# Performance work log

Hardware: AMD Instinct MI355X
Metric: run time of the kernel (lower is better)

The kernel has to match this reference:

```python
import jax, jax.numpy as jnp
import numpy as np

B, T, K, D, H, HL, S, KN = 4096, 50, 32, 64, 256, 128, 100000, 1000


def setup_inputs() -> dict:
    key = jax.random.key(0)
    ks = jax.random.split(key, 24)
    inp = {
        "uididx": jax.random.randint(ks[0], (B,), 0, S, dtype=jnp.int32),
        "kcodeidx": jax.random.randint(ks[1], (B, K), 0, KN, dtype=jnp.int32),
        "kcode_len": jax.random.randint(ks[2], (B,), 1, K + 1, dtype=jnp.int32),
        "qidemb": jax.random.normal(ks[3], (B, T, D), dtype=jnp.float32),
        "qid_len": jax.random.randint(ks[4], (B,), 1, T + 1, dtype=jnp.int32),
        # embedding tables
        "stuE": jax.random.normal(ks[5], (S, D), dtype=jnp.float32) * 0.1,
        "knE": jax.random.normal(ks[6], (KN, D), dtype=jnp.float32) * 0.1,
        # Theta DNN params
        "T_W1": jax.random.normal(ks[7], (D, H), dtype=jnp.float32) * (1.0 / np.sqrt(D)),
        "T_b1": jnp.zeros((H,), jnp.float32),
        "T_W2": jax.random.normal(ks[8], (H, 1), dtype=jnp.float32) * (1.0 / np.sqrt(H)),
        "T_b2": jnp.zeros((1,), jnp.float32),
        # A DNN params
        "A_W1": jax.random.normal(ks[9], (D, H), dtype=jnp.float32) * (1.0 / np.sqrt(D)),
        "A_b1": jnp.zeros((H,), jnp.float32),
        "A_W2": jax.random.normal(ks[10], (H, 1), dtype=jnp.float32) * (1.0 / np.sqrt(H)),
        "A_b2": jnp.zeros((1,), jnp.float32),
        # LSTM params (gate order i,f,g,o) + output head
        "L_Wi": jax.random.normal(ks[11], (D, 4 * HL), dtype=jnp.float32) * (1.0 / np.sqrt(D)),
        "L_Wh": jax.random.normal(ks[12], (HL, 4 * HL), dtype=jnp.float32) * (1.0 / np.sqrt(HL)),
        "L_b": jnp.zeros((4 * HL,), jnp.float32),
        "L_Wo": jax.random.normal(ks[13], (HL, 1), dtype=jnp.float32) * (1.0 / np.sqrt(HL)),
        "L_bo": jnp.zeros((1,), jnp.float32),
    }
    return inp


def _dnn(x, W1, b1, W2, b2):
    return jnp.tanh(x @ W1 + b1) @ W2 + b2


def _lstm_last(x, lengths, Wi, Wh, b):
    # x: [B,T,D]; returns last valid hidden state [B,HL]
    xg = jnp.einsum('btd,dh->bth', x, Wi) + b  # precomputed input projections
    h0 = jnp.zeros((x.shape[0], Wh.shape[0]), x.dtype)

    def step(carry, inp):
        h, c = carry
        g_x, t = inp
        g = g_x + h @ Wh
        i, f, gg, o = jnp.split(g, 4, axis=-1)
        c2 = jax.nn.sigmoid(f) * c + jax.nn.sigmoid(i) * jnp.tanh(gg)
        h2 = jax.nn.sigmoid(o) * jnp.tanh(c2)
        upd = (t < lengths)[:, None]
        return (jnp.where(upd, h2, h), jnp.where(upd, c2, c)), None

    (h, _), _ = jax.lax.scan(step, (h0, h0), (xg.transpose(1, 0, 2), jnp.arange(x.shape[1])))
    return h


def reference(uididx, kcodeidx, kcode_len, qidemb, qid_len, stuE, knE,
              T_W1, T_b1, T_W2, T_b2, A_W1, A_b1, A_W2, A_b2,
              L_Wi, L_Wh, L_b, L_Wo, L_bo):
    stu = stuE[uididx]            # [B,D]
    kemb = knE[kcodeidx]          # [B,K,D]
    kmask = jnp.arange(kcodeidx.shape[1])[None, :] < kcode_len[:, None]  # [B,K]
    kmf = kmask.astype(kemb.dtype)

    # per-student mastery: sigmoid(kemb @ stu / 5), then masked reductions
    mastery = jax.nn.sigmoid(jnp.einsum('bkd,bd->bk', kemb, stu) / 5.0)
    mastvec = jnp.einsum('bk,bkd->bd', mastery * kmf, kemb)  # sum(mastery * kemb)
    avec = jnp.einsum('bk,bkd->bd', kmf, kemb)               # sum(kemb)

    # scaled dot-product attention: q=qidemb, k=v=kemb, scale=0.15
    scores = jnp.einsum('btd,bkd->btk', qidemb, kemb) * 0.15
    scores = jnp.where(kmask[:, None, :], scores, -1e9)
    attw = jax.nn.softmax(scores, axis=-1)
    bvec = jnp.einsum('btk,bkd->btd', attw, kemb)            # [B,T,D]

    t = _dnn(mastvec, T_W1, T_b1, T_W2, T_b2)                             # theta [B,1]
    a = 8.0 * (jax.nn.sigmoid(jnp.abs(_dnn(avec, A_W1, A_b1, A_W2, A_b2))) - 0.5)
    hT = _lstm_last(bvec, qid_len, L_Wi, L_Wh, L_b)
    b = 8.0 * (jax.nn.sigmoid(hT @ L_Wo + L_bo) - 0.5)                    # [B,1]

    return jax.nn.sigmoid(a * (t - b))  # IRT response probability [B,1]
```

## Files before the change

### kernel.cpp

```cpp
#include <hip/hip_runtime.h>
#include <math.h>

#define B_  4096
#define T_  50
#define K_  32
#define D_  64
#define H_  256
#define HL_ 128
#define G4_ 512

typedef __attribute__((ext_vector_type(8))) short bf16x8;
typedef __attribute__((ext_vector_type(4))) float f32x4;

__device__ __forceinline__ float fast_exp(float x){ return __expf(x); }
__device__ __forceinline__ float fast_rcp(float x){ return __builtin_amdgcn_rcpf(x); }
__device__ __forceinline__ float sigmoidf_(float x){ return fast_rcp(1.f + fast_exp(-x)); }
__device__ __forceinline__ float tanhf_(float x){ return 1.f - 2.f*fast_rcp(1.f + fast_exp(2.f*x)); }

__device__ __forceinline__ short f2bf(float f){
  union { float f; unsigned u; } v; v.f = f;
  unsigned r = v.u + 0x7FFFu + ((v.u >> 16) & 1u);
  return (short)(r >> 16);
}
__device__ __forceinline__ float bf2f(short s){
  union { unsigned u; float f; } v; v.u = ((unsigned)(unsigned short)s) << 16;
  return v.f;
}

__device__ __forceinline__ float wave_reduce_sum(float v){
  #pragma unroll
  for (int off = 32; off; off >>= 1) v += __shfl_xor(v, off);
  return v;
}

#define KROW 72
#define PROW 40

__global__ __launch_bounds__(256) void head_kernel(
    const int* __restrict__ uididx, const int* __restrict__ kcodeidx,
    const int* __restrict__ kcode_len, const float* __restrict__ qidemb,
    const int* __restrict__ qid_len, const float* __restrict__ stuE,
    const float* __restrict__ knE,
    const float* __restrict__ T_W1, const float* __restrict__ T_b1,
    const float* __restrict__ T_W2, const float* __restrict__ T_b2,
    const float* __restrict__ A_W1, const float* __restrict__ A_b1,
    const float* __restrict__ A_W2, const float* __restrict__ A_b2,
    short* __restrict__ bvec, float* __restrict__ t_val, float* __restrict__ a_val)
{
  __shared__ __align__(16) short s_kemb[K_*KROW];
  __shared__ __align__(16) short s_kembT[D_*PROW];
  __shared__ __align__(16) short s_p[64*PROW];
  __shared__ float s_stu[D_];
  __shared__ float s_mast[K_];
  __shared__ float s_kmf[K_];
  __shared__ float s_mvec[D_];
  __shared__ float s_avec[D_];
  __shared__ float s_redT[4];
  __shared__ float s_redA[4];

  const int b    = blockIdx.x;
  const int tid  = threadIdx.x;
  const int lane = tid & 63;
  const int w    = tid >> 6;
  const int l15  = lane & 15;
  const int quad = lane >> 4;
  const int klen = kcode_len[b];
  const int qlen = qid_len[b];

  if (tid < D_) s_stu[tid] = stuE[uididx[b]*D_ + tid];
  #pragma unroll
  for (int i = tid; i < 512; i += 256){
    int k = i >> 4, f4 = i & 15;
    const float4 v = *(const float4*)&knE[(size_t)kcodeidx[b*K_ + k]*D_ + f4*4];
    short4 b4; b4.x = f2bf(v.x); b4.y = f2bf(v.y); b4.z = f2bf(v.z); b4.w = f2bf(v.w);
    *(short4*)&s_kemb[k*KROW + f4*4] = b4;
    int d = f4*4;
    s_kembT[(d+0)*PROW + k] = b4.x;
    s_kembT[(d+1)*PROW + k] = b4.y;
    s_kembT[(d+2)*PROW + k] = b4.z;
    s_kembT[(d+3)*PROW + k] = b4.w;
  }
  __syncthreads();

  {
    int k = tid >> 3, l8 = tid & 7;
    float s = 0.f;
    #pragma unroll
    for (int j = 0; j < 8; ++j){
      int d = l8 + 8*((j + k) & 7);
      s += s_stu[d] * bf2f(s_kemb[k*KROW + d]);
    }
    s += __shfl_xor(s, 1); s += __shfl_xor(s, 2); s += __shfl_xor(s, 4);
    if (l8 == 0){
      float valid = (k < klen) ? 1.f : 0.f;
      s_mast[k] = valid * sigmoidf_(s * 0.2f);
      s_kmf[k]  = valid;
    }
  }
  __syncthreads();

  if (tid < D_){
    float mv = 0.f, av = 0.f;
    #pragma unroll 4
    for (int k = 0; k < K_; ++k){
      float e = bf2f(s_kemb[k*KROW + tid]);
      mv += s_mast[k] * e;
      av += s_kmf[k]  * e;
    }
    s_mvec[tid] = mv; s_avec[tid] = av;
  }
  __syncthreads();

  {
    const int qrow = w*16 + l15;
    bf16x8 aq[2];
    #pragma unroll
    for (int kt = 0; kt < 2; ++kt){
      if (qrow < qlen){
        const float4 v0 = *(const float4*)&qidemb[((size_t)b*T_ + qrow)*D_ + kt*32 + quad*8];
        const float4 v1 = *(const float4*)&qidemb[((size_t)b*T_ + qrow)*D_ + kt*32 + quad*8 + 4];
        aq[kt][0]=f2bf(v0.x); aq[kt][1]=f2bf(v0.y); aq[kt][2]=f2bf(v0.z); aq[kt][3]=f2bf(v0.w);
        aq[kt][4]=f2bf(v1.x); aq[kt][5]=f2bf(v1.y); aq[kt][6]=f2bf(v1.z); aq[kt][7]=f2bf(v1.w);
      } else {
        aq[kt][0]=0; aq[kt][1]=0; aq[kt][2]=0; aq[kt][3]=0;
        aq[kt][4]=0; aq[kt][5]=0; aq[kt][6]=0; aq[kt][7]=0;
      }
    }
    f32x4 zero = {0.f, 0.f, 0.f, 0.f};
    f32x4 accs[2] = {zero, zero};
    #pragma unroll
    for (int kt = 0; kt < 2; ++kt){
      #pragma unroll
      for (int nt = 0; nt < 2; ++nt){
        bf16x8 bk = *(const bf16x8*)&s_kemb[(nt*16 + l15)*KROW + kt*32 + quad*8];
        accs[nt] = __builtin_amdgcn_mfma_f32_16x16x32_bf16(aq[kt], bk, accs[nt], 0, 0, 0);
      }
    }
    #pragma unroll
    for (int r = 0; r < 4; ++r){
      float v0 = (l15      < klen) ? accs[0][r]*0.15f : -1e9f;
      float v1 = (l15 + 16 < klen) ? accs[1][r]*0.15f : -1e9f;
      float mx = fmaxf(v0, v1);
      #pragma unroll
      for (int off = 1; off < 16; off <<= 1) mx = fmaxf(mx, __shfl_xor(mx, off));
      float e0 = fast_exp(v0 - mx), e1 = fast_exp(v1 - mx);
      float sm = e0 + e1;
      #pragma unroll
      for (int off = 1; off < 16; off <<= 1) sm += __shfl_xor(sm, off);
      float inv = fast_rcp(sm);
      int row = w*16 + quad*4 + r;
      s_p[row*PROW + l15]      = f2bf(e0 * inv);
      s_p[row*PROW + 16 + l15] = f2bf(e1 * inv);
    }
    bf16x8 ap = *(const bf16x8*)&s_p[(w*16 + l15)*PROW + quad*8];
    #pragma unroll
    for (int nt = 0; nt < 4; ++nt){
      bf16x8 bv = *(const bf16x8*)&s_kembT[(nt*16 + l15)*PROW + quad*8];
      f32x4 acco = __builtin_amdgcn_mfma_f32_16x16x32_bf16(ap, bv, zero, 0, 0, 0);
      #pragma unroll
      for (int r = 0; r < 4; ++r){
        int t = w*16 + quad*4 + r;
        if (t < qlen) bvec[((size_t)b*T_ + t)*D_ + nt*16 + l15] = f2bf(acco[r]);
      }
    }
  }

  {
    float accT = T_b1[tid];
    float accA = A_b1[tid];
    #pragma unroll 4
    for (int d = 0; d < D_; ++d){
      float mv = s_mvec[d], av = s_avec[d];
      accT += mv * T_W1[d*H_ + tid];
      accA += av * A_W1[d*H_ + tid];
    }
    float termT = tanhf_(accT) * T_W2[tid];
    float termA = tanhf_(accA) * A_W2[tid];
    termT = wave_reduce_sum(termT);
    termA = wave_reduce_sum(termA);
    if (lane == 0){ s_redT[w] = termT; s_redA[w] = termA; }
    __syncthreads();
    if (tid == 0){
      t_val[b] = s_redT[0] + s_redT[1] + s_redT[2] + s_redT[3] + T_b2[0];
      float v = s_redA[0] + s_redA[1] + s_redA[2] + s_redA[3] + A_b2[0];
      a_val[b] = 8.f * (sigmoidf_(fabsf(v)) - 0.5f);
    }
  }
}

#define AROW 408

__global__ __launch_bounds__(512) void lstm_kernel(
    const short* __restrict__ bvec, const int* __restrict__ qid_len,
    const float* __restrict__ L_Wi, const float* __restrict__ L_Wh,
    const float* __restrict__ L_b,  const float* __restrict__ L_Wo,
    const float* __restrict__ L_bo, const float* __restrict__ t_val,
    const float* __restrict__ a_val, float* __restrict__ out)
{
  __shared__ __align__(16) short s_A[16*AROW];
  __shared__ int s_len[16];

  const int tid  = threadIdx.x;
  const int s0   = blockIdx.x * 16;
  const int w    = tid >> 6;
  const int lane = tid & 63;
  const int l15  = lane & 15;
  const int quad = lane >> 4;

  bf16x8 wf[4][6];
  f32x4  biasv4[4];
  #pragma unroll
  for (int g = 0; g < 4; ++g){
    const int col = g*128 + w*16 + l15;
    #pragma unroll
    for (int r = 0; r < 4; ++r) biasv4[g][r] = L_b[g*128 + w*16 + quad*4 + r];
    #pragma unroll
    for (int kt = 0; kt < 6; ++kt){
      #pragma unroll
      for (int j = 0; j < 8; ++j){
        int k = kt*32 + quad*8 + j;
        float v = (k < D_) ? L_Wi[k*G4_ + col] : L_Wh[(k-D_)*G4_ + col];
        wf[g][kt][j] = f2bf(v);
      }
    }
  }

  for (int p = tid; p < 16*AROW; p += 512) s_A[p] = 0;
  if (tid < 16) s_len[tid] = qid_len[s0 + tid];
  __syncthreads();

  const int xs = tid >> 5, xpos = tid & 31;
  {
    const short2 xv = *(const short2*)&bvec[((size_t)(s0+xs)*T_ + 0)*D_ + xpos*2];
    *(short2*)&s_A[xs*AROW + xpos*2] = xv;
  }
  int maxlen = 0;
  #pragma unroll
  for (int i = 0; i < 16; ++i) maxlen = max(maxlen, s_len[i]);
  const int mylen = s_len[l15];
  float c_reg[4] = {0.f,0.f,0.f,0.f};
  float h_reg[4] = {0.f,0.f,0.f,0.f};

  short2 xv_reg;
  if (1 < maxlen) xv_reg = *(const short2*)&bvec[((size_t)(s0+xs)*T_ + 1)*D_ + xpos*2];
  __syncthreads();

#define LSTM_STEP(TI, XB) do {                                                 \
    const int xb_ = (XB); const int hb_ = xb_ ^ 1;                             \
    if ((TI) + 1 < maxlen) *(short2*)&s_A[xs*AROW + hb_*64 + xpos*2] = xv_reg; \
    if ((TI) + 2 < maxlen)                                                     \
      xv_reg = *(const short2*)&bvec[((size_t)(s0+xs)*T_ + ((TI)+2))*D_ + xpos*2]; \
    bf16x8 af[6];                                                              \
    af[0] = *(const bf16x8*)&s_A[l15*AROW + xb_*64 +      quad*8];             \
    af[1] = *(const bf16x8*)&s_A[l15*AROW + xb_*64 + 32 + quad*8];             \
    _Pragma("unroll")                                                          \
    for (int kt = 0; kt < 4; ++kt)                                             \
      af[2+kt] = *(const bf16x8*)&s_A[l15*AROW + 128 + hb_*128 + kt*32 + quad*8]; \
    f32x4 acc[4];                                                              \
    acc[0]=biasv4[0]; acc[1]=biasv4[1]; acc[2]=biasv4[2]; acc[3]=biasv4[3];    \
    _Pragma("unroll")                                                          \
    for (int kt = 0; kt < 6; ++kt){                                            \
      _Pragma("unroll")                                                        \
      for (int g = 0; g < 4; ++g)                                              \
        acc[g] = __builtin_amdgcn_mfma_f32_16x16x32_bf16(wf[g][kt], af[kt], acc[g], 0, 0, 0); \
    }                                                                          \
    const bool upd_ = (TI) < mylen;                                            \
    _Pragma("unroll")                                                          \
    for (int r = 0; r < 4; ++r){                                               \
      float gi = acc[0][r], gf = acc[1][r], gg = acc[2][r], go = acc[3][r];    \
      float c2 = sigmoidf_(gf)*c_reg[r] + sigmoidf_(gi)*tanhf_(gg);            \
      float h2 = sigmoidf_(go)*tanhf_(c2);                                     \
      c_reg[r] = upd_ ? c2 : c_reg[r];                                         \
      h_reg[r] = upd_ ? h2 : h_reg[r];                                         \
    }                                                                          \
    uint2 hp_;                                                                 \
    hp_.x = (unsigned)(unsigned short)f2bf(h_reg[0])                           \
          | ((unsigned)(unsigned short)f2bf(h_reg[1]) << 16);                  \
    hp_.y = (unsigned)(unsigned short)f2bf(h_reg[2])                           \
          | ((unsigned)(unsigned short)f2bf(h_reg[3]) << 16);                  \
    *(uint2*)&s_A[l15*AROW + 128 + xb_*128 + w*16 + quad*4] = hp_;             \
    __syncthreads();                                                           \
  } while(0)

  int t = 0;
  for (; t + 1 < maxlen; t += 2){
    LSTM_STEP(t,   0);
    LSTM_STEP(t+1, 1);
  }
  if (t < maxlen) LSTM_STEP(t, 0);
#undef LSTM_STEP

  const int xbLast = (maxlen - 1) & 1;
  for (int s2 = w; s2 < 16; s2 += 8){
    float h0 = bf2f(s_A[s2*AROW + 128 + xbLast*128 + lane]);
    float h1 = bf2f(s_A[s2*AROW + 128 + xbLast*128 + 64 + lane]);
    float part = h0*L_Wo[lane] + h1*L_Wo[64+lane];
    part = wave_reduce_sum(part);
    if (lane == 0){
      float bb = 8.f * (sigmoidf_(part + L_bo[0]) - 0.5f);
      out[s0+s2] = sigmoidf_(a_val[s0+s2] * (t_val[s0+s2] - bb));
    }
  }
}

extern "C" void kernel_launch(void* const* d_in, const int* in_sizes, int n_in,
                              void* d_out, int out_size, void* d_ws, size_t ws_size,
                              hipStream_t stream)
{
  (void)in_sizes; (void)n_in; (void)out_size; (void)ws_size;
  const int*   uididx    = (const int*)  d_in[0];
  const int*   kcodeidx  = (const int*)  d_in[1];
  const int*   kcode_len = (const int*)  d_in[2];
  const float* qidemb    = (const float*)d_in[3];
  const int*   qid_len   = (const int*)  d_in[4];
  const float* stuE      = (const float*)d_in[5];
  const float* knE       = (const float*)d_in[6];
  const float* T_W1      = (const float*)d_in[7];
  const float* T_b1      = (const float*)d_in[8];
  const float* T_W2      = (const float*)d_in[9];
  const float* T_b2      = (const float*)d_in[10];
  const float* A_W1      = (const float*)d_in[11];
  const float* A_b1      = (const float*)d_in[12];
  const float* A_W2      = (const float*)d_in[13];
  const float* A_b2      = (const float*)d_in[14];
  const float* L_Wi      = (const float*)d_in[15];
  const float* L_Wh      = (const float*)d_in[16];
  const float* L_b       = (const float*)d_in[17];
  const float* L_Wo      = (const float*)d_in[18];
  const float* L_bo      = (const float*)d_in[19];
  float* out = (float*)d_out;

  short* bvec  = (short*)d_ws;
  float* t_val = (float*)(bvec + (size_t)B_*T_*D_);
  float* a_val = t_val + B_;

  hipLaunchKernelGGL(head_kernel, dim3(B_), dim3(256), 0, stream,
    uididx, kcodeidx, kcode_len, qidemb, qid_len, stuE, knE,
    T_W1, T_b1, T_W2, T_b2, A_W1, A_b1, A_W2, A_b2,
    bvec, t_val, a_val);

  hipLaunchKernelGGL(lstm_kernel, dim3(B_/16), dim3(512), 0, stream,
    bvec, qid_len, L_Wi, L_Wh, L_b, L_Wo, L_bo, t_val, a_val, out);
}
```

Baseline: 221.8 us.

## Load LSTM input fragments directly from global and interleave gate MFMAs with activations

The LSTM kernel no longer stages the per-step input x into shared memory. Each lane now loads its MFMA input fragments straight from global memory into registers, double-buffered two steps ahead, which shrinks the LDS row and removes the x store from each step. The x-projection MFMAs are issued first, before the h-dependent ones, so they can overlap the LDS reads of h. Gate activations are interleaved between the remaining MFMA chains to hide transcendental latency. The cost is more global load traffic per lane (16 rows × 64 elements per wave, duplicated across waves) and higher register pressure.

```diff
diff --git a/kernel.cpp b/kernel.cpp
--- a/kernel.cpp
+++ b/kernel.cpp
@@ -188,7 +188,7 @@
   }
 }
 
-#define AROW 408
+#define HROW 280
 
 __global__ __launch_bounds__(512) void lstm_kernel(
     const short* __restrict__ bvec, const int* __restrict__ qid_len,
@@ -197,7 +197,7 @@
     const float* __restrict__ L_bo, const float* __restrict__ t_val,
     const float* __restrict__ a_val, float* __restrict__ out)
 {
-  __shared__ __align__(16) short s_A[16*AROW];
+  __shared__ __align__(16) short s_A[16*HROW];
   __shared__ int s_len[16];
 
   const int tid  = threadIdx.x;
@@ -225,15 +225,10 @@
     }
   }
 
-  for (int p = tid; p < 16*AROW; p += 512) s_A[p] = 0;
+  for (int p = tid; p < 16*HROW; p += 512) s_A[p] = 0;
   if (tid < 16) s_len[tid] = qid_len[s0 + tid];
   __syncthreads();
 
-  const int xs = tid >> 5, xpos = tid & 31;
-  {
-    const short2 xv = *(const short2*)&bvec[((size_t)(s0+xs)*T_ + 0)*D_ + xpos*2];
-    *(short2*)&s_A[xs*AROW + xpos*2] = xv;
-  }
   int maxlen = 0;
   #pragma unroll
   for (int i = 0; i < 16; ++i) maxlen = max(maxlen, s_len[i]);
@@ -241,35 +236,48 @@
   float c_reg[4] = {0.f,0.f,0.f,0.f};
   float h_reg[4] = {0.f,0.f,0.f,0.f};
 
-  short2 xv_reg;
-  if (1 < maxlen) xv_reg = *(const short2*)&bvec[((size_t)(s0+xs)*T_ + 1)*D_ + xpos*2];
-  __syncthreads();
-
-#define LSTM_STEP(TI, XB) do {                                                 \
-    const int xb_ = (XB); const int hb_ = xb_ ^ 1;                             \
-    if ((TI) + 1 < maxlen) *(short2*)&s_A[xs*AROW + hb_*64 + xpos*2] = xv_reg; \
-    if ((TI) + 2 < maxlen)                                                     \
-      xv_reg = *(const short2*)&bvec[((size_t)(s0+xs)*T_ + ((TI)+2))*D_ + xpos*2]; \
-    bf16x8 af[6];                                                              \
-    af[0] = *(const bf16x8*)&s_A[l15*AROW + xb_*64 +      quad*8];             \
-    af[1] = *(const bf16x8*)&s_A[l15*AROW + xb_*64 + 32 + quad*8];             \
-    _Pragma("unroll")                                                          \
-    for (int kt = 0; kt < 4; ++kt)                                             \
-      af[2+kt] = *(const bf16x8*)&s_A[l15*AROW + 128 + hb_*128 + kt*32 + quad*8]; \
-    f32x4 acc[4];                                                              \
-    acc[0]=biasv4[0]; acc[1]=biasv4[1]; acc[2]=biasv4[2]; acc[3]=biasv4[3];    \
-    _Pragma("unroll")                                                          \
-    for (int kt = 0; kt < 6; ++kt){                                            \
-      _Pragma("unroll")                                                        \
-      for (int g = 0; g < 4; ++g)                                              \
-        acc[g] = __builtin_amdgcn_mfma_f32_16x16x32_bf16(wf[g][kt], af[kt], acc[g], 0, 0, 0); \
+  const short* gx = bvec + (size_t)(s0 + l15)*T_*D_ + quad*8;
+  bf16x8 xA0 = *(const bf16x8*)(gx);
+  bf16x8 xA1 = *(const bf16x8*)(gx + 32);
+  bf16x8 xB0 = xA0, xB1 = xA1;
+  if (1 < maxlen){ xB0 = *(const bf16x8*)(gx + D_); xB1 = *(const bf16x8*)(gx + D_ + 32); }
+  __syncthreads();
+
+#define MF(Aop, Bop, Cop) __builtin_amdgcn_mfma_f32_16x16x32_bf16((Aop), (Bop), (Cop), 0, 0, 0)
+
+#define LSTM_STEP(TI, XB, XC0, XC1) do {                                       \
+    const int hb_ = (XB) ^ 1;                                                  \
+    const bf16x8 ah0 = *(const bf16x8*)&s_A[l15*HROW + hb_*128 +  0 + quad*8]; \
+    const bf16x8 ah1 = *(const bf16x8*)&s_A[l15*HROW + hb_*128 + 32 + quad*8]; \
+    const bf16x8 ah2 = *(const bf16x8*)&s_A[l15*HROW + hb_*128 + 64 + quad*8]; \
+    const bf16x8 ah3 = *(const bf16x8*)&s_A[l15*HROW + hb_*128 + 96 + quad*8]; \
+    f32x4 a0_ = biasv4[0], a1_ = biasv4[1], a2_ = biasv4[2], a3_ = biasv4[3];  \
+    a0_ = MF(wf[0][0], XC0, a0_); a0_ = MF(wf[0][1], XC1, a0_);                \
+    a1_ = MF(wf[1][0], XC0, a1_); a1_ = MF(wf[1][1], XC1, a1_);                \
+    a2_ = MF(wf[2][0], XC0, a2_); a2_ = MF(wf[2][1], XC1, a2_);                \
+    a3_ = MF(wf[3][0], XC0, a3_); a3_ = MF(wf[3][1], XC1, a3_);                \
+    if ((TI) + 2 < maxlen){                                                    \
+      XC0 = *(const bf16x8*)(gx + ((TI)+2)*D_);                                \
+      XC1 = *(const bf16x8*)(gx + ((TI)+2)*D_ + 32);                           \
     }                                                                          \
+    a0_ = MF(wf[0][2], ah0, a0_); a0_ = MF(wf[0][3], ah1, a0_);                \
+    a0_ = MF(wf[0][4], ah2, a0_); a0_ = MF(wf[0][5], ah3, a0_);                \
+    a1_ = MF(wf[1][2], ah0, a1_); a1_ = MF(wf[1][3], ah1, a1_);                \
+    a1_ = MF(wf[1][4], ah2, a1_); a1_ = MF(wf[1][5], ah3, a1_);                \
+    float si_[4], sf_[4], tg_[4], so_[4];                                      \
+    _Pragma("unroll") for (int r = 0; r < 4; ++r) si_[r] = sigmoidf_(a0_[r]);  \
+    a2_ = MF(wf[2][2], ah0, a2_); a2_ = MF(wf[2][3], ah1, a2_);                \
+    a2_ = MF(wf[2][4], ah2, a2_); a2_ = MF(wf[2][5], ah3, a2_);                \
+    _Pragma("unroll") for (int r = 0; r < 4; ++r) sf_[r] = sigmoidf_(a1_[r]);  \
+    a3_ = MF(wf[3][2], ah0, a3_); a3_ = MF(wf[3][3], ah1, a3_);                \
+    a3_ = MF(wf[3][4], ah2, a3_); a3_ = MF(wf[3][5], ah3, a3_);                \
+    _Pragma("unroll") for (int r = 0; r < 4; ++r) tg_[r] = tanhf_(a2_[r]);     \
+    _Pragma("unroll") for (int r = 0; r < 4; ++r) so_[r] = sigmoidf_(a3_[r]);  \
     const bool upd_ = (TI) < mylen;                                            \
     _Pragma("unroll")                                                          \
     for (int r = 0; r < 4; ++r){                                               \
-      float gi = acc[0][r], gf = acc[1][r], gg = acc[2][r], go = acc[3][r];    \
-      float c2 = sigmoidf_(gf)*c_reg[r] + sigmoidf_(gi)*tanhf_(gg);            \
-      float h2 = sigmoidf_(go)*tanhf_(c2);                                     \
+      float c2 = sf_[r]*c_reg[r] + si_[r]*tg_[r];                              \
+      float h2 = so_[r]*tanhf_(c2);                                            \
       c_reg[r] = upd_ ? c2 : c_reg[r];                                         \
       h_reg[r] = upd_ ? h2 : h_reg[r];                                         \
     }                                                                          \
@@ -278,22 +286,23 @@
           | ((unsigned)(unsigned short)f2bf(h_reg[1]) << 16);                  \
     hp_.y = (unsigned)(unsigned short)f2bf(h_reg[2])                           \
           | ((unsigned)(unsigned short)f2bf(h_reg[3]) << 16);                  \
-    *(uint2*)&s_A[l15*AROW + 128 + xb_*128 + w*16 + quad*4] = hp_;             \
+    *(uint2*)&s_A[l15*HROW + (XB)*128 + w*16 + quad*4] = hp_;                  \
     __syncthreads();                                                           \
   } while(0)
 
   int t = 0;
   for (; t + 1 < maxlen; t += 2){
-    LSTM_STEP(t,   0);
-    LSTM_STEP(t+1, 1);
-  }
-  if (t < maxlen) LSTM_STEP(t, 0);
+    LSTM_STEP(t,   0, xA0, xA1);
+    LSTM_STEP(t+1, 1, xB0, xB1);
+  }
+  if (t < maxlen) LSTM_STEP(t, 0, xA0, xA1);
 #undef LSTM_STEP
+#undef MF
 
   const int xbLast = (maxlen - 1) & 1;
   for (int s2 = w; s2 < 16; s2 += 8){
-    float h0 = bf2f(s_A[s2*AROW + 128 + xbLast*128 + lane]);
-    float h1 = bf2f(s_A[s2*AROW + 128 + xbLast*128 + 64 + lane]);
+    float h0 = bf2f(s_A[s2*HROW + xbLast*128 + lane]);
+    float h1 = bf2f(s_A[s2*HROW + xbLast*128 + 64 + lane]);
     float part = h0*L_Wo[lane] + h1*L_Wo[64+lane];
     part = wave_reduce_sum(part);
     if (lane == 0){
```

Result: no change. 219.1 us (-1.2%).
